# Optimization experiments

Measured on AMD Instinct MI355X. Metric: run time of the kernel, lower is better.

Reference implementation:

```python
import jax, jax.numpy as jnp
import numpy as np

B, N, E = 4, 10000, 160000
F_EXOG = 8
IN_DIM = 9          # 1 (pm25) + F_EXOG
HIST, PRED = 8, 12
HID = 64
GNN_OUT = 13
E_HID, E_OUT = 32, 30
GRU_IN = IN_DIM + GNN_OUT  # 22


def setup_inputs() -> dict:
    key = jax.random.key(0)
    ks = jax.random.split(key, 16)
    s = 0.1
    return {
        "pm25_hist": jax.random.normal(ks[0], (B, HIST, N, 1), jnp.float32),
        "feature": jax.random.normal(ks[1], (B, HIST + PRED, N, F_EXOG), jnp.float32),
        "edge_attr": jax.random.uniform(ks[2], (E, 2), jnp.float32),
        "wind_mean": jnp.array([2.0, 180.0], jnp.float32),
        "wind_std": jnp.array([1.5, 90.0], jnp.float32),
        # edge MLP: Linear(21->32), Sigmoid, Linear(32->30), Sigmoid
        "e_w1": jax.random.normal(ks[3], (2 * IN_DIM + 3, E_HID), jnp.float32) * s,
        "e_b1": jnp.zeros((E_HID,), jnp.float32),
        "e_w2": jax.random.normal(ks[4], (E_HID, E_OUT), jnp.float32) * s,
        "e_b2": jnp.zeros((E_OUT,), jnp.float32),
        # node MLP: Linear(30->13), Sigmoid
        "n_w": jax.random.normal(ks[5], (E_OUT, GNN_OUT), jnp.float32) * s,
        "n_b": jnp.zeros((GNN_OUT,), jnp.float32),
        # GRUCell(22 -> 64), torch layout: weight_ih (3H, in), weight_hh (3H, H)
        "gru_wi": jax.random.normal(ks[6], (3 * HID, GRU_IN), jnp.float32) * s,
        "gru_wh": jax.random.normal(ks[7], (3 * HID, HID), jnp.float32) * s,
        "gru_bi": jnp.zeros((3 * HID,), jnp.float32),
        "gru_bh": jnp.zeros((3 * HID,), jnp.float32),
        # fc_out: Linear(64 -> 1)
        "fc_w": jax.random.normal(ks[8], (HID, 1), jnp.float32) * s,
        "fc_b": jnp.zeros((1,), jnp.float32),
        "edge_index": jax.random.randint(ks[9], (2, E), 0, N, jnp.int64),
    }


def _forward(pm25_hist, feature, edge_attr, wind_mean, wind_std,
             e_w1, e_b1, e_w2, e_b2, n_w, n_b,
             gru_wi, gru_wh, gru_bi, gru_bh, fc_w, fc_b, edge_index):
    batch, _, n_nodes, _ = pm25_hist.shape
    src, tgt = edge_index[0], edge_index[1]

    # buffers precomputed in __init__ (torch.std uses ddof=1)
    edge_mean = edge_attr.mean(axis=0, keepdims=True)
    edge_std = jnp.maximum(jnp.std(edge_attr, axis=0, ddof=1, keepdims=True), 1e-6)
    edge_attr_norm = (edge_attr - edge_mean) / edge_std          # (E, 2)
    city_dist = jnp.maximum(edge_attr[:, 0], 1e-3)               # (E,)
    city_direc = edge_attr[:, 1]                                 # (E,)
    w_std = jnp.maximum(wind_std, 1e-6)

    def graph_gnn(x):                                            # x: (B, N, IN_DIM)
        node_src = x[:, src]                                     # (B, E, IN_DIM)
        node_tgt = x[:, tgt]
        wind = node_src[..., -2:] * w_std + wind_mean            # de-normalize
        speed = jnp.maximum(wind[..., 0], 0.0)                   # (B, E)
        wdir = jnp.deg2rad(wind[..., 1])
        theta = jnp.abs(city_direc - wdir)
        edge_w = jax.nn.relu(3.0 * speed * jnp.cos(theta) / city_dist)  # (B, E)
        ean = jnp.broadcast_to(edge_attr_norm, (x.shape[0], E, 2))
        h = jnp.concatenate([node_src, node_tgt, ean, edge_w[..., None]], axis=-1)
        h = jax.nn.sigmoid(h @ e_w1 + e_b1)
        h = jax.nn.sigmoid(h @ e_w2 + e_b2)                      # (B, E, E_OUT)
        agg = jnp.zeros((x.shape[0], n_nodes, E_OUT), x.dtype)
        agg = agg.at[:, tgt].add(h).at[:, src].add(-h)           # scatter add / sub
        return jax.nn.sigmoid(agg @ n_w + n_b)                   # (B, N, GNN_OUT)

    def gru_step(h, x):                                          # h,x: (B*N, .)
        gi = x @ gru_wi.T + gru_bi
        gh = h @ gru_wh.T + gru_bh
        i_r, i_z, i_n = jnp.split(gi, 3, axis=-1)
        h_r, h_z, h_n = jnp.split(gh, 3, axis=-1)
        r = jax.nn.sigmoid(i_r + h_r)
        z = jax.nn.sigmoid(i_z + h_z)
        n = jnp.tanh(i_n + r * h_n)
        return (1.0 - z) * n + z * h

    def step(carry, feat_t):
        hn, xn = carry                                           # (B*N,HID), (B,N,1)
        x = jnp.concatenate([xn, feat_t], axis=-1)               # (B, N, IN_DIM)
        x_gnn = graph_gnn(x)
        xc = jnp.concatenate([x_gnn, x], axis=-1).reshape(batch * n_nodes, -1)
        hn = gru_step(hn, xc)
        xn = hn.reshape(batch, n_nodes, HID) @ fc_w + fc_b       # (B, N, 1)
        return (hn, xn), xn[..., 0]

    hn0 = jnp.zeros((batch * n_nodes, HID), pm25_hist.dtype)
    xn0 = pm25_hist[:, -1]                                       # (B, N, 1)
    feats = jnp.swapaxes(feature[:, HIST:HIST + PRED], 0, 1)     # (PRED, B, N, F)
    _, preds = jax.lax.scan(step, (hn0, xn0), feats)             # (PRED, B, N)
    return jnp.transpose(preds, (1, 2, 0))                       # (B, N, PRED)


def reference(pm25_hist, feature, edge_attr, wind_mean, wind_std,
              e_w1, e_b1, e_w2, e_b2, n_w, n_b,
              gru_wi, gru_wh, gru_bi, gru_bh, fc_w, fc_b, edge_index):
    return _forward(pm25_hist, feature, edge_attr, wind_mean, wind_std,
                    e_w1, e_b1, e_w2, e_b2, n_w, n_b,
                    gru_wi, gru_wh, gru_bi, gru_bh, fc_w, fc_b, edge_index)
```

## Files before the change

### kernel.cpp

```cpp
#include <hip/hip_runtime.h>
#include <hip/hip_fp16.h>
#include <cstddef>

#define BB    4
#define NN    10000
#define EE    160000
#define BN    40000
#define HISTC 8
#define PREDC 12
#define TSTEP 20
#define FEX   8
#define HIDC  64
#define EHID  32
#define EOUTC 30
#define GOUTC 13
#define GINC  22

typedef float v2f __attribute__((ext_vector_type(2)));
typedef _Float16 v2h __attribute__((ext_vector_type(2)));

struct alignas(16) WPack {
    __half2 w[16];
    float   nw[14];
    float   b2;
    float   pad;
};

__device__ __forceinline__ float fast_rcp(float x) { return __builtin_amdgcn_rcpf(x); }
__device__ __forceinline__ float sigm(float x) {
    return fast_rcp(1.0f + __expf(-x));
}
__device__ __forceinline__ v2f sigm2(v2f x) {
    v2f r; r.x = sigm(x.x); r.y = sigm(x.y); return r;
}
__device__ __forceinline__ float tanh_fast(float x) {
    x = fminf(fmaxf(x, -15.0f), 15.0f);
    float e = __expf(2.0f * x);
    return (e - 1.0f) * fast_rcp(e + 1.0f);
}

__device__ __forceinline__ float dot2(__half2 a, __half2 b, float c) {
#if __has_builtin(__builtin_amdgcn_fdot2)
    union { __half2 h; v2h v; } ua, ub;
    ua.h = a; ub.h = b;
    return __builtin_amdgcn_fdot2(ua.v, ub.v, c, false);
#else
    float2 fa = __half22float2(a), fb = __half22float2(b);
    return c + fa.x * fb.x + fa.y * fb.y;
#endif
}

__global__ __launch_bounds__(256) void stats1_kernel(const float* __restrict__ ea,
                                                     double* __restrict__ part) {
    __shared__ double sm[256][4];
    int tid = threadIdx.x;
    double s0 = 0, s1 = 0, q0 = 0, q1 = 0;
    for (int e = blockIdx.x * 256 + tid; e < EE; e += 256 * 256) {
        float2 v = reinterpret_cast<const float2*>(ea)[e];
        double v0 = (double)v.x, v1 = (double)v.y;
        s0 += v0; q0 += v0 * v0;
        s1 += v1; q1 += v1 * v1;
    }
    sm[tid][0] = s0; sm[tid][1] = s1; sm[tid][2] = q0; sm[tid][3] = q1;
    __syncthreads();
    for (int off = 128; off > 0; off >>= 1) {
        if (tid < off)
            for (int k = 0; k < 4; k++) sm[tid][k] += sm[tid + off][k];
        __syncthreads();
    }
    if (tid == 0) {
        part[blockIdx.x * 4 + 0] = sm[0][0];
        part[blockIdx.x * 4 + 1] = sm[0][1];
        part[blockIdx.x * 4 + 2] = sm[0][2];
        part[blockIdx.x * 4 + 3] = sm[0][3];
    }
}

__global__ __launch_bounds__(256) void stats2_kernel(const double* __restrict__ part,
                                                     float* __restrict__ stats) {
    __shared__ double sm[256][4];
    int tid = threadIdx.x;
    sm[tid][0] = part[tid * 4 + 0];
    sm[tid][1] = part[tid * 4 + 1];
    sm[tid][2] = part[tid * 4 + 2];
    sm[tid][3] = part[tid * 4 + 3];
    __syncthreads();
    for (int off = 128; off > 0; off >>= 1) {
        if (tid < off)
            for (int k = 0; k < 4; k++) sm[tid][k] += sm[tid + off][k];
        __syncthreads();
    }
    if (tid == 0) {
        double m0 = sm[0][0] / EE, m1 = sm[0][1] / EE;
        double v0 = (sm[0][2] - sm[0][0] * sm[0][0] / EE) / (double)(EE - 1);
        double v1 = (sm[0][3] - sm[0][1] * sm[0][1] / EE) / (double)(EE - 1);
        float sd0 = fmaxf((float)sqrt(v0 > 0 ? v0 : 0.0), 1e-6f);
        float sd1 = fmaxf((float)sqrt(v1 > 0 ? v1 : 0.0), 1e-6f);
        stats[0] = (float)m0; stats[1] = (float)m1;
        stats[2] = 1.0f / sd0; stats[3] = 1.0f / sd1;
    }
}

__global__ __launch_bounds__(256) void edgepre_kernel(
    const float* __restrict__ ea, const float* __restrict__ stats,
    const int* __restrict__ eidx,
    int* __restrict__ deg_t, int* __restrict__ deg_s,
    float4* __restrict__ epre4)
{
    int e = blockIdx.x * 256 + threadIdx.x;
    if (e >= EE) return;
    float2 v = reinterpret_cast<const float2*>(ea)[e];
    float4 r;
    r.x = (v.x - stats[0]) * stats[2];
    r.y = (v.y - stats[1]) * stats[3];
    r.z = 1.0f / fmaxf(v.x, 1e-3f);
    r.w = v.y;
    epre4[e] = r;
    atomicAdd(&deg_s[eidx[e]], 1);
    atomicAdd(&deg_t[eidx[EE + e]], 1);
}

__global__ __launch_bounds__(256) void cvtw_kernel(
    const float* __restrict__ wi, const float* __restrict__ wh,
    const float* __restrict__ ew2, const float* __restrict__ eb2,
    const float* __restrict__ nw,
    __half* __restrict__ wi_h, __half* __restrict__ wh_h,
    WPack* __restrict__ wpack)
{
    int i = blockIdx.x * 256 + threadIdx.x;
    if (i < 192 * GINC) wi_h[i] = __float2half(wi[i]);
    if (i < 192 * HIDC) wh_h[i] = __float2half(wh[i]);
    if (i < EOUTC) {
        WPack wp;
        #pragma unroll
        for (int q = 0; q < 16; q++)
            wp.w[q] = __floats2half2_rn(ew2[(2 * q) * EOUTC + i],
                                        ew2[(2 * q + 1) * EOUTC + i]);
        #pragma unroll
        for (int j = 0; j < GOUTC; j++) wp.nw[j] = nw[i * GOUTC + j];
        wp.nw[13] = 0.f;
        wp.b2 = eb2[i];
        wp.pad = 0.f;
        wpack[i] = wp;
    }
}

__global__ void initxn_kernel(const float* __restrict__ pm, float* __restrict__ xn) {
    int i = blockIdx.x * 256 + threadIdx.x;
    if (i >= BN) return;
    int b = i / NN, n = i - b * NN;
    xn[i] = pm[(b * HISTC + (HISTC - 1)) * NN + n];
}

__global__ __launch_bounds__(1024) void scan_kernel(
    const int* __restrict__ deg_t, const int* __restrict__ deg_s,
    int* __restrict__ off_t, int* __restrict__ off_s,
    int* __restrict__ cnt_t, int* __restrict__ cnt_s)
{
    __shared__ int pt[1024], ps[1024];
    int tid = threadIdx.x;
    int base = tid * 10;
    int st = 0, ss = 0;
    for (int k = 0; k < 10; k++) {
        int i = base + k;
        if (i < NN) { st += deg_t[i]; ss += deg_s[i]; }
    }
    pt[tid] = st; ps[tid] = ss;
    __syncthreads();
    for (int off = 1; off < 1024; off <<= 1) {
        int vt = (tid >= off) ? pt[tid - off] : 0;
        int vs = (tid >= off) ? ps[tid - off] : 0;
        __syncthreads();
        pt[tid] += vt; ps[tid] += vs;
        __syncthreads();
    }
    int ext = (tid == 0) ? 0 : pt[tid - 1];
    int exs = (tid == 0) ? 0 : ps[tid - 1];
    for (int k = 0; k < 10; k++) {
        int i = base + k;
        if (i < NN) {
            off_t[i] = ext; cnt_t[i] = ext;
            off_s[i] = exs; cnt_s[i] = exs;
            ext += deg_t[i]; exs += deg_s[i];
        }
    }
    if (tid == 0) { off_t[NN] = EE; off_s[NN] = EE; }
}

__global__ void fillperm_kernel(const int* __restrict__ eidx,
                                const float4* __restrict__ epre4,
                                int* __restrict__ cnt_t, int* __restrict__ cnt_s,
                                int4* __restrict__ eT, float4* __restrict__ epreT)
{
    int e = blockIdx.x * 256 + threadIdx.x;
    if (e >= EE) return;
    int s = eidx[e];
    int g = eidx[EE + e];
    int pt = atomicAdd(&cnt_t[g], 1);
    int ps = atomicAdd(&cnt_s[s], 1);
    int4 r; r.x = s; r.y = g; r.z = ps; r.w = 0;
    eT[pt] = r;
    epreT[pt] = epre4[e];
}

__global__ __launch_bounds__(256) void pre_kernel(
    float* __restrict__ xncur, const float* __restrict__ feature, int t,
    const float* __restrict__ xp,
    const float* __restrict__ fb,
    const float* __restrict__ ew1,
    const float* __restrict__ wmean, const float* __restrict__ wstd,
    __half* __restrict__ preS, __half* __restrict__ preT,
    float2* __restrict__ wind2, float* __restrict__ out)
{
    __shared__ alignas(16) float w1s[18 * EHID];
    for (int i = threadIdx.x; i < 18 * EHID; i += 256) w1s[i] = ew1[i];
    __syncthreads();
    int idx = blockIdx.x * 256 + threadIdx.x;
    if (idx >= BN * 8) return;
    int i = idx >> 3;
    int c = idx & 7;
    int b = i / NN, n = i - b * NN;
    float x0;
    if (t == 0) {
        x0 = xncur[i];
    } else {
        x0 = (xp[i] + xp[BN + i]) + (xp[2 * BN + i] + xp[3 * BN + i]) + fb[0];
        if (c == 0) {
            xncur[i] = x0;
            out[(size_t)i * PREDC + (t - 1)] = x0;
        }
    }
    float x[9];
    x[0] = x0;
    {
        const float4* fp = reinterpret_cast<const float4*>(
            feature + (((size_t)b * TSTEP + HISTC + t) * NN + n) * FEX);
        float4 u = fp[0], v = fp[1];
        x[1] = u.x; x[2] = u.y; x[3] = u.z; x[4] = u.w;
        x[5] = v.x; x[6] = v.y; x[7] = v.z; x[8] = v.w;
    }
    float4 aS = {0.f, 0.f, 0.f, 0.f}, aT = {0.f, 0.f, 0.f, 0.f};
    #pragma unroll
    for (int k = 0; k < 9; k++) {
        float4 wS = reinterpret_cast<const float4*>(&w1s[k * EHID])[c];
        float4 wT = reinterpret_cast<const float4*>(&w1s[(9 + k) * EHID])[c];
        aS.x += x[k] * wS.x; aS.y += x[k] * wS.y; aS.z += x[k] * wS.z; aS.w += x[k] * wS.w;
        aT.x += x[k] * wT.x; aT.y += x[k] * wT.y; aT.z += x[k] * wT.z; aT.w += x[k] * wT.w;
    }
    union { uint2 u; __half h[4]; } sv, tv;
    sv.h[0] = __float2half(aS.x); sv.h[1] = __float2half(aS.y);
    sv.h[2] = __float2half(aS.z); sv.h[3] = __float2half(aS.w);
    tv.h[0] = __float2half(aT.x); tv.h[1] = __float2half(aT.y);
    tv.h[2] = __float2half(aT.z); tv.h[3] = __float2half(aT.w);
    reinterpret_cast<uint2*>(preS + (size_t)i * EHID)[c] = sv.u;
    reinterpret_cast<uint2*>(preT + (size_t)i * EHID)[c] = tv.u;
    if (c == 1) {
        float sd0 = fmaxf(wstd[0], 1e-6f), sd1 = fmaxf(wstd[1], 1e-6f);
        float speed = fmaxf(x[7] * sd0 + wmean[0], 0.f);
        float wdir  = (x[8] * sd1 + wmean[1]) * 0.017453292519943295f;
        float2 wv; wv.x = 3.0f * speed; wv.y = wdir;
        wind2[i] = wv;
    }
}

__global__ __launch_bounds__(256) void finalout_kernel(
    const float* __restrict__ xp, const float* __restrict__ fb,
    float* __restrict__ out)
{
    int i = blockIdx.x * 256 + threadIdx.x;
    if (i >= BN) return;
    out[(size_t)i * PREDC + (PREDC - 1)] =
        (xp[i] + xp[BN + i]) + (xp[2 * BN + i] + xp[3 * BN + i]) + fb[0];
}

__global__ __launch_bounds__(256) void edge_kernel(
    const int4* __restrict__ eT, const float4* __restrict__ epreT,
    const __half* __restrict__ preS, const __half* __restrict__ preT,
    const float2* __restrict__ wind2,
    const float* __restrict__ ew1, const float* __restrict__ eb1,
    const WPack* __restrict__ wpack,
    __half* __restrict__ h3t, __half* __restrict__ h3s)
{
    int i = blockIdx.x * 256 + threadIdx.x;
    int b = blockIdx.y;
    int4 et = eT[i];
    int s = et.x, g = et.y, ps = et.z;
    float4 ep = epreT[i];

    size_t iS = (size_t)b * NN + s, iT = (size_t)b * NN + g;
    float2 wv2 = wind2[iS];
    float ew = fmaxf(wv2.x * __cosf(fabsf(ep.w - wv2.y)) * ep.z, 0.f);

    union alignas(16) { uint4 u[4]; __half2 h2[16]; } RS, RT;
    {
        const uint4* p;
        p = reinterpret_cast<const uint4*>(preS + iS * EHID);
        RS.u[0] = p[0]; RS.u[1] = p[1]; RS.u[2] = p[2]; RS.u[3] = p[3];
        p = reinterpret_cast<const uint4*>(preT + iT * EHID);
        RT.u[0] = p[0]; RT.u[1] = p[1]; RT.u[2] = p[2]; RT.u[3] = p[3];
    }

    const v2f* W18 = reinterpret_cast<const v2f*>(ew1 + 18 * EHID);
    const v2f* W19 = reinterpret_cast<const v2f*>(ew1 + 19 * EHID);
    const v2f* W20 = reinterpret_cast<const v2f*>(ew1 + 20 * EHID);
    const v2f* B1  = reinterpret_cast<const v2f*>(eb1);
    float ean0 = ep.x, ean1 = ep.y;
    __half2 h1h[16];
    #pragma unroll
    for (int q = 0; q < 16; q++) {
        v2f u = W18[q] * ean0 + W19[q] * ean1 + B1[q] + W20[q] * ew;
        float2 rs = __half22float2(RS.h2[q]);
        float2 rt = __half22float2(RT.h2[q]);
        u.x += rs.x + rt.x;
        u.y += rs.y + rt.y;
        v2f sg = sigm2(u);
        h1h[q] = __floats2half2_rn(sg.x, sg.y);
    }

    v2f h3p[7];
    #pragma unroll
    for (int j = 0; j < 7; j++) { h3p[j].x = 0.f; h3p[j].y = 0.f; }
    for (int o = 0; o < EOUTC; o++) {
        const WPack* W = wpack + o;
        float acc0 = W->b2, acc1 = 0.f;
        #pragma unroll
        for (int q = 0; q < 16; q += 2) {
            acc0 = dot2(h1h[q],     W->w[q],     acc0);
            acc1 = dot2(h1h[q + 1], W->w[q + 1], acc1);
        }
        float h2v = sigm(acc0 + acc1);
        const v2f* nr = reinterpret_cast<const v2f*>(W->nw);
        #pragma unroll
        for (int j = 0; j < 7; j++) h3p[j] += nr[j] * h2v;
    }

    union alignas(16) { uint4 u[2]; __half2 h2[8]; } r;
    #pragma unroll
    for (int j = 0; j < 7; j++) r.h2[j] = __floats2half2_rn(h3p[j].x, h3p[j].y);
    r.h2[7] = __floats2half2_rn(0.f, 0.f);
    {
        __half* oT = h3t + ((size_t)b * EE + i) * 16;
        reinterpret_cast<uint4*>(oT)[0] = r.u[0];
        reinterpret_cast<uint4*>(oT)[1] = r.u[1];
        __half* oS = h3s + ((size_t)b * EE + ps) * 16;
        reinterpret_cast<uint4*>(oS)[0] = r.u[0];
        reinterpret_cast<uint4*>(oS)[1] = r.u[1];
    }
}

__global__ __launch_bounds__(256) void gather_kernel(
    const __half* __restrict__ h3t, const __half* __restrict__ h3s,
    const int* __restrict__ off_t, const int* __restrict__ off_s,
    const float* __restrict__ nb, const float* __restrict__ xncur,
    __half* __restrict__ xcagg)
{
    int n = (blockIdx.x * 256 + threadIdx.x) >> 6;
    if (n >= NN) return;
    n = __builtin_amdgcn_readfirstlane(n);
    int lane = threadIdx.x & 63;
    int b = lane >> 4, ch = lane & 15;
    const __half* ht = h3t + (size_t)b * EE * 16 + ch;
    const __half* hs = h3s + (size_t)b * EE * 16 + ch;
    float a0 = 0.f, a1 = 0.f, a2 = 0.f, a3 = 0.f;
    {
        int i0 = off_t[n], i1 = off_t[n + 1];
        int i = i0;
        for (; i + 4 <= i1; i += 4) {
            a0 += __half2float(ht[(size_t)(i + 0) * 16]);
            a1 += __half2float(ht[(size_t)(i + 1) * 16]);
            a2 += __half2float(ht[(size_t)(i + 2) * 16]);
            a3 += __half2float(ht[(size_t)(i + 3) * 16]);
        }
        for (; i < i1; i++) a0 += __half2float(ht[(size_t)i * 16]);
    }
    {
        int i0 = off_s[n], i1 = off_s[n + 1];
        int i = i0;
        for (; i + 4 <= i1; i += 4) {
            a0 -= __half2float(hs[(size_t)(i + 0) * 16]);
            a1 -= __half2float(hs[(size_t)(i + 1) * 16]);
            a2 -= __half2float(hs[(size_t)(i + 2) * 16]);
            a3 -= __half2float(hs[(size_t)(i + 3) * 16]);
        }
        for (; i < i1; i++) a0 -= __half2float(hs[(size_t)i * 16]);
    }
    float acc = (a0 + a1) + (a2 + a3);
    float val;
    if (ch < GOUTC) {
        val = sigm(acc + nb[ch]);
    } else if (ch == GOUTC) {
        val = xncur[(size_t)b * NN + n];
    } else {
        val = 0.f;
    }
    xcagg[((size_t)b * NN + n) * 16 + ch] = __float2half(val);
}

__global__ __launch_bounds__(256) void node_kernel(
    const __half* __restrict__ xcagg, const float* __restrict__ feature, int t,
    const __half* __restrict__ wi_h, const __half* __restrict__ wh_h,
    const float* __restrict__ bi, const float* __restrict__ bh,
    const float* __restrict__ fw,
    const __half2* __restrict__ hnold, __half2* __restrict__ hnnew,
    float* __restrict__ xp)
{
    __shared__ float xpart[4][64];
    int lane = threadIdx.x & 63;
    int wav  = threadIdx.x >> 6;
    int jb   = blockIdx.y;
    int node = blockIdx.x * 64 + lane;
    int b = node / NN;
    int n = node - b * NN;

    __half2 xch[11];
    {
        union alignas(16) { uint4 u[2]; __half2 h2[8]; } X;
        const uint4* xp16 = reinterpret_cast<const uint4*>(xcagg + (size_t)node * 16);
        X.u[0] = xp16[0]; X.u[1] = xp16[1];
        #pragma unroll
        for (int p = 0; p < 7; p++) xch[p] = X.h2[p];
    }
    {
        const float4* fp = reinterpret_cast<const float4*>(
            feature + (((size_t)b * TSTEP + HISTC + t) * NN + n) * FEX);
        float4 u = fp[0], v = fp[1];
        xch[7]  = __floats2half2_rn(u.x, u.y);
        xch[8]  = __floats2half2_rn(u.z, u.w);
        xch[9]  = __floats2half2_rn(v.x, v.y);
        xch[10] = __floats2half2_rn(v.z, v.w);
    }

    __half2 hh[32];
    #pragma unroll
    for (int p = 0; p < 32; p++) hh[p] = hnold[(size_t)p * BN + node];

    float xsum = 0.f;
    #pragma unroll
    for (int jj2 = 0; jj2 < 2; jj2++) {
        int j0 = __builtin_amdgcn_readfirstlane(jb * 16 + wav * 4 + jj2 * 2);
        union { __half2 h; __half v[2]; } holdw;
        holdw.h = hnold[(size_t)(j0 >> 1) * BN + node];
        float hnew2[2];
        #pragma unroll
        for (int d = 0; d < 2; d++) {
            int j = j0 + d;
            float ir = bi[j], iz = bi[64 + j], in_ = bi[128 + j];
            const __half2* wr0 = reinterpret_cast<const __half2*>(wi_h + (size_t)j * GINC);
            const __half2* wr1 = reinterpret_cast<const __half2*>(wi_h + (size_t)(64 + j) * GINC);
            const __half2* wr2 = reinterpret_cast<const __half2*>(wi_h + (size_t)(128 + j) * GINC);
            #pragma unroll
            for (int p = 0; p < 11; p++) {
                ir  = dot2(xch[p], wr0[p], ir);
                iz  = dot2(xch[p], wr1[p], iz);
                in_ = dot2(xch[p], wr2[p], in_);
            }
            float hr0 = bh[j], hz0 = bh[64 + j], hn0 = bh[128 + j];
            float hr1 = 0.f, hz1 = 0.f, hn1 = 0.f;
            const __half2* vr0 = reinterpret_cast<const __half2*>(wh_h + (size_t)j * HIDC);
            const __half2* vr1 = reinterpret_cast<const __half2*>(wh_h + (size_t)(64 + j) * HIDC);
            const __half2* vr2 = reinterpret_cast<const __half2*>(wh_h + (size_t)(128 + j) * HIDC);
            #pragma unroll
            for (int p = 0; p < 32; p += 2) {
                hr0 = dot2(hh[p],     vr0[p],     hr0);
                hz0 = dot2(hh[p],     vr1[p],     hz0);
                hn0 = dot2(hh[p],     vr2[p],     hn0);
                hr1 = dot2(hh[p + 1], vr0[p + 1], hr1);
                hz1 = dot2(hh[p + 1], vr1[p + 1], hz1);
                hn1 = dot2(hh[p + 1], vr2[p + 1], hn1);
            }
            float r  = sigm(ir + hr0 + hr1);
            float z  = sigm(iz + hz0 + hz1);
            float nn = tanh_fast(in_ + r * (hn0 + hn1));
            float hold = __half2float(holdw.v[d]);
            float hnew = (1.f - z) * nn + z * hold;
            hnew2[d] = hnew;
            xsum += hnew * fw[j];
        }
        hnnew[(size_t)(j0 >> 1) * BN + node] = __floats2half2_rn(hnew2[0], hnew2[1]);
    }
    xpart[wav][lane] = xsum;
    __syncthreads();
    if (wav == 0) {
        float tot = xpart[0][lane] + xpart[1][lane] + xpart[2][lane] + xpart[3][lane];
        xp[(size_t)jb * BN + node] = tot;
    }
}

extern "C" void kernel_launch(void* const* d_in, const int* in_sizes, int n_in,
                              void* d_out, int out_size, void* d_ws, size_t ws_size,
                              hipStream_t stream)
{
    const float* pm    = (const float*)d_in[0];
    const float* feat  = (const float*)d_in[1];
    const float* ea    = (const float*)d_in[2];
    const float* wmean = (const float*)d_in[3];
    const float* wstd  = (const float*)d_in[4];
    const float* ew1   = (const float*)d_in[5];
    const float* eb1   = (const float*)d_in[6];
    const float* ew2   = (const float*)d_in[7];
    const float* eb2   = (const float*)d_in[8];
    const float* nw    = (const float*)d_in[9];
    const float* nb    = (const float*)d_in[10];
    const float* wi    = (const float*)d_in[11];
    const float* wh    = (const float*)d_in[12];
    const float* bi    = (const float*)d_in[13];
    const float* bh    = (const float*)d_in[14];
    const float* fw    = (const float*)d_in[15];
    const float* fb    = (const float*)d_in[16];
    const int*   eidx  = (const int*)d_in[17];
    float* out = (float*)d_out;

    char* w = (char*)d_ws;
    double* partd = (double*)w;                    w += 256 * 4 * sizeof(double);
    float*  stats = (float*)w;                     w += 16 * sizeof(float);
    WPack*  wpack = (WPack*)w;                     w += EOUTC * sizeof(WPack);
    float4* epre4 = (float4*)w;                    w += (size_t)EE * sizeof(float4);
    float4* epreT = (float4*)w;                    w += (size_t)EE * sizeof(float4);
    float*  xncur = (float*)w;                     w += (size_t)BN * sizeof(float);
    float*  xp    = (float*)w;                     w += (size_t)4 * BN * sizeof(float);
    __half2* hnA  = (__half2*)w;                   w += (size_t)32 * BN * sizeof(__half2);
    __half2* hnB  = (__half2*)w;                   w += (size_t)32 * BN * sizeof(__half2);
    __half* xcagg = (__half*)w;                    w += (size_t)BN * 16 * sizeof(__half);
    __half* preS  = (__half*)w;                    w += (size_t)BN * EHID * sizeof(__half);
    __half* preT  = (__half*)w;                    w += (size_t)BN * EHID * sizeof(__half);
    float2* wind2 = (float2*)w;                    w += (size_t)BN * sizeof(float2);
    __half* h3t   = (__half*)w;                    w += (size_t)BB * EE * 16 * sizeof(__half);
    __half* h3s   = (__half*)w;                    w += (size_t)BB * EE * 16 * sizeof(__half);
    __half* wi_h  = (__half*)w;                    w += (size_t)192 * GINC * sizeof(__half);
    __half* wh_h  = (__half*)w;                    w += (size_t)192 * HIDC * sizeof(__half);
    int*    deg_t = (int*)w;                       w += NN * sizeof(int);
    int*    deg_s = (int*)w;                       w += NN * sizeof(int);
    int*    off_t = (int*)w;                       w += (NN + 1) * sizeof(int);
    int*    off_s = (int*)w;                       w += (NN + 1) * sizeof(int);
    int*    cnt_t = (int*)w;                       w += NN * sizeof(int);
    int*    cnt_s = (int*)w;                       w += NN * sizeof(int);
    int4*   eT    = (int4*)w;                      w += (size_t)EE * sizeof(int4);

    stats1_kernel<<<256, 256, 0, stream>>>(ea, partd);
    stats2_kernel<<<1, 256, 0, stream>>>(partd, stats);
    hipMemsetAsync(deg_t, 0, 2 * NN * sizeof(int), stream);
    edgepre_kernel<<<(EE + 255) / 256, 256, 0, stream>>>(
        ea, stats, eidx, deg_t, deg_s, epre4);
    cvtw_kernel<<<(192 * HIDC + 255) / 256, 256, 0, stream>>>(
        wi, wh, ew2, eb2, nw, wi_h, wh_h, wpack);
    initxn_kernel<<<(BN + 255) / 256, 256, 0, stream>>>(pm, xncur);
    hipMemsetAsync(hnA, 0, (size_t)32 * BN * sizeof(__half2), stream);
    scan_kernel<<<1, 1024, 0, stream>>>(deg_t, deg_s, off_t, off_s, cnt_t, cnt_s);
    fillperm_kernel<<<(EE + 255) / 256, 256, 0, stream>>>(
        eidx, epre4, cnt_t, cnt_s, eT, epreT);

    for (int t = 0; t < PREDC; t++) {
        const __half2* hnold = (t & 1) ? hnB : hnA;
        __half2*       hnnew = (t & 1) ? hnA : hnB;
        pre_kernel<<<(BN * 8 + 255) / 256, 256, 0, stream>>>(
            xncur, feat, t, xp, fb, ew1, wmean, wstd, preS, preT, wind2, out);
        edge_kernel<<<dim3(EE / 256, BB), 256, 0, stream>>>(
            eT, epreT, preS, preT, wind2, ew1, eb1, wpack, h3t, h3s);
        gather_kernel<<<(NN * 64 + 255) / 256, 256, 0, stream>>>(
            h3t, h3s, off_t, off_s, nb, xncur, xcagg);
        node_kernel<<<dim3(BN / 64, 4), 256, 0, stream>>>(
            xcagg, feat, t, wi_h, wh_h, bi, bh, fw, hnold, hnnew, xp);
    }
    finalout_kernel<<<(BN + 255) / 256, 256, 0, stream>>>(xp, fb, out);
}
```

Baseline: 1.046 ms.

## Precompute feature edge-MLP terms for all steps and fuse gather with GRU node step

```diff
diff --git a/kernel.cpp b/kernel.cpp
--- a/kernel.cpp
+++ b/kernel.cpp
@@ -203,80 +203,61 @@
     epreT[pt] = epre4[e];
 }
 
-__global__ __launch_bounds__(256) void pre_kernel(
-    float* __restrict__ xncur, const float* __restrict__ feature, int t,
-    const float* __restrict__ xp,
-    const float* __restrict__ fb,
+__global__ __launch_bounds__(256) void featpre_kernel(
+    const float* __restrict__ feature,
     const float* __restrict__ ew1,
     const float* __restrict__ wmean, const float* __restrict__ wstd,
-    __half* __restrict__ preS, __half* __restrict__ preT,
-    float2* __restrict__ wind2, float* __restrict__ out)
+    __half* __restrict__ preSfeat, __half* __restrict__ preTfeat,
+    float2* __restrict__ wind2all)
 {
     __shared__ alignas(16) float w1s[18 * EHID];
     for (int i = threadIdx.x; i < 18 * EHID; i += 256) w1s[i] = ew1[i];
     __syncthreads();
     int idx = blockIdx.x * 256 + threadIdx.x;
-    if (idx >= BN * 8) return;
-    int i = idx >> 3;
-    int c = idx & 7;
+    if (idx >= BN * 8 * PREDC) return;
+    int c  = idx & 7;
+    int r2 = idx >> 3;
+    int t  = r2 / BN;
+    int i  = r2 - t * BN;
     int b = i / NN, n = i - b * NN;
-    float x0;
-    if (t == 0) {
-        x0 = xncur[i];
-    } else {
-        x0 = (xp[i] + xp[BN + i]) + (xp[2 * BN + i] + xp[3 * BN + i]) + fb[0];
-        if (c == 0) {
-            xncur[i] = x0;
-            out[(size_t)i * PREDC + (t - 1)] = x0;
-        }
-    }
-    float x[9];
-    x[0] = x0;
+    float xf[8];
     {
         const float4* fp = reinterpret_cast<const float4*>(
             feature + (((size_t)b * TSTEP + HISTC + t) * NN + n) * FEX);
         float4 u = fp[0], v = fp[1];
-        x[1] = u.x; x[2] = u.y; x[3] = u.z; x[4] = u.w;
-        x[5] = v.x; x[6] = v.y; x[7] = v.z; x[8] = v.w;
+        xf[0] = u.x; xf[1] = u.y; xf[2] = u.z; xf[3] = u.w;
+        xf[4] = v.x; xf[5] = v.y; xf[6] = v.z; xf[7] = v.w;
     }
     float4 aS = {0.f, 0.f, 0.f, 0.f}, aT = {0.f, 0.f, 0.f, 0.f};
     #pragma unroll
-    for (int k = 0; k < 9; k++) {
-        float4 wS = reinterpret_cast<const float4*>(&w1s[k * EHID])[c];
-        float4 wT = reinterpret_cast<const float4*>(&w1s[(9 + k) * EHID])[c];
-        aS.x += x[k] * wS.x; aS.y += x[k] * wS.y; aS.z += x[k] * wS.z; aS.w += x[k] * wS.w;
-        aT.x += x[k] * wT.x; aT.y += x[k] * wT.y; aT.z += x[k] * wT.z; aT.w += x[k] * wT.w;
+    for (int k = 0; k < 8; k++) {
+        float4 wS = reinterpret_cast<const float4*>(&w1s[(k + 1) * EHID])[c];
+        float4 wT = reinterpret_cast<const float4*>(&w1s[(10 + k) * EHID])[c];
+        aS.x += xf[k] * wS.x; aS.y += xf[k] * wS.y; aS.z += xf[k] * wS.z; aS.w += xf[k] * wS.w;
+        aT.x += xf[k] * wT.x; aT.y += xf[k] * wT.y; aT.z += xf[k] * wT.z; aT.w += xf[k] * wT.w;
     }
     union { uint2 u; __half h[4]; } sv, tv;
     sv.h[0] = __float2half(aS.x); sv.h[1] = __float2half(aS.y);
     sv.h[2] = __float2half(aS.z); sv.h[3] = __float2half(aS.w);
     tv.h[0] = __float2half(aT.x); tv.h[1] = __float2half(aT.y);
     tv.h[2] = __float2half(aT.z); tv.h[3] = __float2half(aT.w);
-    reinterpret_cast<uint2*>(preS + (size_t)i * EHID)[c] = sv.u;
-    reinterpret_cast<uint2*>(preT + (size_t)i * EHID)[c] = tv.u;
+    size_t base = ((size_t)t * BN + i) * EHID;
+    reinterpret_cast<uint2*>(preSfeat + base)[c] = sv.u;
+    reinterpret_cast<uint2*>(preTfeat + base)[c] = tv.u;
     if (c == 1) {
         float sd0 = fmaxf(wstd[0], 1e-6f), sd1 = fmaxf(wstd[1], 1e-6f);
-        float speed = fmaxf(x[7] * sd0 + wmean[0], 0.f);
-        float wdir  = (x[8] * sd1 + wmean[1]) * 0.017453292519943295f;
+        float speed = fmaxf(xf[6] * sd0 + wmean[0], 0.f);
+        float wdir  = (xf[7] * sd1 + wmean[1]) * 0.017453292519943295f;
         float2 wv; wv.x = 3.0f * speed; wv.y = wdir;
-        wind2[i] = wv;
-    }
-}
-
-__global__ __launch_bounds__(256) void finalout_kernel(
-    const float* __restrict__ xp, const float* __restrict__ fb,
-    float* __restrict__ out)
-{
-    int i = blockIdx.x * 256 + threadIdx.x;
-    if (i >= BN) return;
-    out[(size_t)i * PREDC + (PREDC - 1)] =
-        (xp[i] + xp[BN + i]) + (xp[2 * BN + i] + xp[3 * BN + i]) + fb[0];
+        wind2all[(size_t)t * BN + i] = wv;
+    }
 }
 
 __global__ __launch_bounds__(256) void edge_kernel(
     const int4* __restrict__ eT, const float4* __restrict__ epreT,
-    const __half* __restrict__ preS, const __half* __restrict__ preT,
-    const float2* __restrict__ wind2,
+    const __half* __restrict__ preSfeat, const __half* __restrict__ preTfeat,
+    const float2* __restrict__ wind2all, int t,
+    const float* __restrict__ xncur,
     const float* __restrict__ ew1, const float* __restrict__ eb1,
     const WPack* __restrict__ wpack,
     __half* __restrict__ h3t, __half* __restrict__ h3s)
@@ -288,18 +269,22 @@
     float4 ep = epreT[i];
 
     size_t iS = (size_t)b * NN + s, iT = (size_t)b * NN + g;
-    float2 wv2 = wind2[iS];
+    size_t tb = (size_t)t * BN;
+    float2 wv2 = wind2all[tb + iS];
     float ew = fmaxf(wv2.x * __cosf(fabsf(ep.w - wv2.y)) * ep.z, 0.f);
+    float xnS = xncur[iS], xnT = xncur[iT];
 
     union alignas(16) { uint4 u[4]; __half2 h2[16]; } RS, RT;
     {
         const uint4* p;
-        p = reinterpret_cast<const uint4*>(preS + iS * EHID);
+        p = reinterpret_cast<const uint4*>(preSfeat + (tb + iS) * EHID);
         RS.u[0] = p[0]; RS.u[1] = p[1]; RS.u[2] = p[2]; RS.u[3] = p[3];
-        p = reinterpret_cast<const uint4*>(preT + iT * EHID);
+        p = reinterpret_cast<const uint4*>(preTfeat + (tb + iT) * EHID);
         RT.u[0] = p[0]; RT.u[1] = p[1]; RT.u[2] = p[2]; RT.u[3] = p[3];
     }
 
+    const v2f* W00 = reinterpret_cast<const v2f*>(ew1);
+    const v2f* W09 = reinterpret_cast<const v2f*>(ew1 + 9 * EHID);
     const v2f* W18 = reinterpret_cast<const v2f*>(ew1 + 18 * EHID);
     const v2f* W19 = reinterpret_cast<const v2f*>(ew1 + 19 * EHID);
     const v2f* W20 = reinterpret_cast<const v2f*>(ew1 + 20 * EHID);
@@ -308,7 +293,8 @@
     __half2 h1h[16];
     #pragma unroll
     for (int q = 0; q < 16; q++) {
-        v2f u = W18[q] * ean0 + W19[q] * ean1 + B1[q] + W20[q] * ew;
+        v2f u = W18[q] * ean0 + W19[q] * ean1 + B1[q] + W20[q] * ew
+              + W00[q] * xnS + W09[q] * xnT;
         float2 rs = __half22float2(RS.h2[q]);
         float2 rt = __half22float2(RT.h2[q]);
         u.x += rs.x + rt.x;
@@ -348,81 +334,77 @@
     }
 }
 
-__global__ __launch_bounds__(256) void gather_kernel(
+__global__ __launch_bounds__(256) void gathernode_kernel(
     const __half* __restrict__ h3t, const __half* __restrict__ h3s,
     const int* __restrict__ off_t, const int* __restrict__ off_s,
-    const float* __restrict__ nb, const float* __restrict__ xncur,
-    __half* __restrict__ xcagg)
-{
-    int n = (blockIdx.x * 256 + threadIdx.x) >> 6;
-    if (n >= NN) return;
-    n = __builtin_amdgcn_readfirstlane(n);
-    int lane = threadIdx.x & 63;
-    int b = lane >> 4, ch = lane & 15;
-    const __half* ht = h3t + (size_t)b * EE * 16 + ch;
-    const __half* hs = h3s + (size_t)b * EE * 16 + ch;
-    float a0 = 0.f, a1 = 0.f, a2 = 0.f, a3 = 0.f;
-    {
-        int i0 = off_t[n], i1 = off_t[n + 1];
-        int i = i0;
-        for (; i + 4 <= i1; i += 4) {
-            a0 += __half2float(ht[(size_t)(i + 0) * 16]);
-            a1 += __half2float(ht[(size_t)(i + 1) * 16]);
-            a2 += __half2float(ht[(size_t)(i + 2) * 16]);
-            a3 += __half2float(ht[(size_t)(i + 3) * 16]);
-        }
-        for (; i < i1; i++) a0 += __half2float(ht[(size_t)i * 16]);
-    }
-    {
-        int i0 = off_s[n], i1 = off_s[n + 1];
-        int i = i0;
-        for (; i + 4 <= i1; i += 4) {
-            a0 -= __half2float(hs[(size_t)(i + 0) * 16]);
-            a1 -= __half2float(hs[(size_t)(i + 1) * 16]);
-            a2 -= __half2float(hs[(size_t)(i + 2) * 16]);
-            a3 -= __half2float(hs[(size_t)(i + 3) * 16]);
-        }
-        for (; i < i1; i++) a0 -= __half2float(hs[(size_t)i * 16]);
-    }
-    float acc = (a0 + a1) + (a2 + a3);
-    float val;
-    if (ch < GOUTC) {
-        val = sigm(acc + nb[ch]);
-    } else if (ch == GOUTC) {
-        val = xncur[(size_t)b * NN + n];
-    } else {
-        val = 0.f;
-    }
-    xcagg[((size_t)b * NN + n) * 16 + ch] = __float2half(val);
-}
-
-__global__ __launch_bounds__(256) void node_kernel(
-    const __half* __restrict__ xcagg, const float* __restrict__ feature, int t,
+    const float* __restrict__ nb,
+    const float* __restrict__ feature, int t,
     const __half* __restrict__ wi_h, const __half* __restrict__ wh_h,
     const float* __restrict__ bi, const float* __restrict__ bh,
-    const float* __restrict__ fw,
+    const float* __restrict__ fw, const float* __restrict__ fb,
     const __half2* __restrict__ hnold, __half2* __restrict__ hnnew,
-    float* __restrict__ xp)
-{
+    float* __restrict__ xncur, float* __restrict__ out)
+{
+    __shared__ alignas(16) __half xcs[16][4][16];
     __shared__ float xpart[4][64];
-    int lane = threadIdx.x & 63;
-    int wav  = threadIdx.x >> 6;
-    int jb   = blockIdx.y;
-    int node = blockIdx.x * 64 + lane;
-    int b = node / NN;
-    int n = node - b * NN;
+    int tid = threadIdx.x;
+    int n0 = blockIdx.x * 16;
+
+    {
+        int l = tid & 63;
+        int gb = l >> 4, ch = l & 15;
+        int wv = tid >> 6;
+        const __half* ht = h3t + (size_t)gb * ((size_t)EE * 16) + ch;
+        const __half* hs = h3s + (size_t)gb * ((size_t)EE * 16) + ch;
+        for (int rr = 0; rr < 4; rr++) {
+            int ln = rr * 4 + wv;
+            int n = __builtin_amdgcn_readfirstlane(n0 + ln);
+            float a0 = 0.f, a1 = 0.f, a2 = 0.f, a3 = 0.f;
+            {
+                int i0 = off_t[n], i1 = off_t[n + 1];
+                int i = i0;
+                for (; i + 4 <= i1; i += 4) {
+                    a0 += __half2float(ht[(size_t)(i + 0) * 16]);
+                    a1 += __half2float(ht[(size_t)(i + 1) * 16]);
+                    a2 += __half2float(ht[(size_t)(i + 2) * 16]);
+                    a3 += __half2float(ht[(size_t)(i + 3) * 16]);
+                }
+                for (; i < i1; i++) a0 += __half2float(ht[(size_t)i * 16]);
+            }
+            {
+                int i0 = off_s[n], i1 = off_s[n + 1];
+                int i = i0;
+                for (; i + 4 <= i1; i += 4) {
+                    a0 -= __half2float(hs[(size_t)(i + 0) * 16]);
+                    a1 -= __half2float(hs[(size_t)(i + 1) * 16]);
+                    a2 -= __half2float(hs[(size_t)(i + 2) * 16]);
+                    a3 -= __half2float(hs[(size_t)(i + 3) * 16]);
+                }
+                for (; i < i1; i++) a0 -= __half2float(hs[(size_t)i * 16]);
+            }
+            float acc = (a0 + a1) + (a2 + a3);
+            __half v = (ch < GOUTC) ? __float2half(sigm(acc + nb[ch]))
+                                    : __float2half(0.f);
+            xcs[ln][gb][ch] = v;
+        }
+    }
+    __syncthreads();
+
+    int lane = tid & 63, wav = tid >> 6;
+    int nn = lane & 15, b = lane >> 4;
+    int node = b * NN + n0 + nn;
+    float xn_old = xncur[node];
 
     __half2 xch[11];
     {
-        union alignas(16) { uint4 u[2]; __half2 h2[8]; } X;
-        const uint4* xp16 = reinterpret_cast<const uint4*>(xcagg + (size_t)node * 16);
-        X.u[0] = xp16[0]; X.u[1] = xp16[1];
+        const __half2* xp2 = reinterpret_cast<const __half2*>(&xcs[nn][b][0]);
         #pragma unroll
-        for (int p = 0; p < 7; p++) xch[p] = X.h2[p];
+        for (int p = 0; p < 6; p++) xch[p] = xp2[p];
+        xch[6] = __halves2half2(xcs[nn][b][12], __float2half(xn_old));
     }
     {
         const float4* fp = reinterpret_cast<const float4*>(
-            feature + (((size_t)b * TSTEP + HISTC + t) * NN + n) * FEX);
+            feature + (((size_t)b * TSTEP + HISTC + t) * NN + (n0 + nn)) * FEX);
         float4 u = fp[0], v = fp[1];
         xch[7]  = __floats2half2_rn(u.x, u.y);
         xch[8]  = __floats2half2_rn(u.z, u.w);
@@ -435,54 +417,58 @@
     for (int p = 0; p < 32; p++) hh[p] = hnold[(size_t)p * BN + node];
 
     float xsum = 0.f;
-    #pragma unroll
-    for (int jj2 = 0; jj2 < 2; jj2++) {
-        int j0 = __builtin_amdgcn_readfirstlane(jb * 16 + wav * 4 + jj2 * 2);
-        union { __half2 h; __half v[2]; } holdw;
-        holdw.h = hnold[(size_t)(j0 >> 1) * BN + node];
-        float hnew2[2];
+    for (int jb = 0; jb < 4; jb++) {
         #pragma unroll
-        for (int d = 0; d < 2; d++) {
-            int j = j0 + d;
-            float ir = bi[j], iz = bi[64 + j], in_ = bi[128 + j];
-            const __half2* wr0 = reinterpret_cast<const __half2*>(wi_h + (size_t)j * GINC);
-            const __half2* wr1 = reinterpret_cast<const __half2*>(wi_h + (size_t)(64 + j) * GINC);
-            const __half2* wr2 = reinterpret_cast<const __half2*>(wi_h + (size_t)(128 + j) * GINC);
+        for (int jj2 = 0; jj2 < 2; jj2++) {
+            int j0 = __builtin_amdgcn_readfirstlane(jb * 16 + wav * 4 + jj2 * 2);
+            union { __half2 h; __half v[2]; } holdw;
+            holdw.h = hnold[(size_t)(j0 >> 1) * BN + node];
+            float hnew2[2];
             #pragma unroll
-            for (int p = 0; p < 11; p++) {
-                ir  = dot2(xch[p], wr0[p], ir);
-                iz  = dot2(xch[p], wr1[p], iz);
-                in_ = dot2(xch[p], wr2[p], in_);
+            for (int d = 0; d < 2; d++) {
+                int j = j0 + d;
+                float ir = bi[j], iz = bi[64 + j], in_ = bi[128 + j];
+                const __half2* wr0 = reinterpret_cast<const __half2*>(wi_h + (size_t)j * GINC);
+                const __half2* wr1 = reinterpret_cast<const __half2*>(wi_h + (size_t)(64 + j) * GINC);
+                const __half2* wr2 = reinterpret_cast<const __half2*>(wi_h + (size_t)(128 + j) * GINC);
+                #pragma unroll
+                for (int p = 0; p < 11; p++) {
+                    ir  = dot2(xch[p], wr0[p], ir);
+                    iz  = dot2(xch[p], wr1[p], iz);
+                    in_ = dot2(xch[p], wr2[p], in_);
+                }
+                float hr0 = bh[j], hz0 = bh[64 + j], hn0 = bh[128 + j];
+                float hr1 = 0.f, hz1 = 0.f, hn1 = 0.f;
+                const __half2* vr0 = reinterpret_cast<const __half2*>(wh_h + (size_t)j * HIDC);
+                const __half2* vr1 = reinterpret_cast<const __half2*>(wh_h + (size_t)(64 + j) * HIDC);
+                const __half2* vr2 = reinterpret_cast<const __half2*>(wh_h + (size_t)(128 + j) * HIDC);
+                #pragma unroll
+                for (int p = 0; p < 32; p += 2) {
+                    hr0 = dot2(hh[p],     vr0[p],     hr0);
+                    hz0 = dot2(hh[p],     vr1[p],     hz0);
+                    hn0 = dot2(hh[p],     vr2[p],     hn0);
+                    hr1 = dot2(hh[p + 1], vr0[p + 1], hr1);
+                    hz1 = dot2(hh[p + 1], vr1[p + 1], hz1);
+                    hn1 = dot2(hh[p + 1], vr2[p + 1], hn1);
+                }
+                float r  = sigm(ir + hr0 + hr1);
+                float z  = sigm(iz + hz0 + hz1);
+                float nl = tanh_fast(in_ + r * (hn0 + hn1));
+                float hold = __half2float(holdw.v[d]);
+                float hnew = (1.f - z) * nl + z * hold;
+                hnew2[d] = hnew;
+                xsum += hnew * fw[j];
             }
-            float hr0 = bh[j], hz0 = bh[64 + j], hn0 = bh[128 + j];
-            float hr1 = 0.f, hz1 = 0.f, hn1 = 0.f;
-            const __half2* vr0 = reinterpret_cast<const __half2*>(wh_h + (size_t)j * HIDC);
-            const __half2* vr1 = reinterpret_cast<const __half2*>(wh_h + (size_t)(64 + j) * HIDC);
-            const __half2* vr2 = reinterpret_cast<const __half2*>(wh_h + (size_t)(128 + j) * HIDC);
-            #pragma unroll
-            for (int p = 0; p < 32; p += 2) {
-                hr0 = dot2(hh[p],     vr0[p],     hr0);
-                hz0 = dot2(hh[p],     vr1[p],     hz0);
-                hn0 = dot2(hh[p],     vr2[p],     hn0);
-                hr1 = dot2(hh[p + 1], vr0[p + 1], hr1);
-                hz1 = dot2(hh[p + 1], vr1[p + 1], hz1);
-                hn1 = dot2(hh[p + 1], vr2[p + 1], hn1);
-            }
-            float r  = sigm(ir + hr0 + hr1);
-            float z  = sigm(iz + hz0 + hz1);
-            float nn = tanh_fast(in_ + r * (hn0 + hn1));
-            float hold = __half2float(holdw.v[d]);
-            float hnew = (1.f - z) * nn + z * hold;
-            hnew2[d] = hnew;
-            xsum += hnew * fw[j];
+            hnnew[(size_t)(j0 >> 1) * BN + node] = __floats2half2_rn(hnew2[0], hnew2[1]);
         }
-        hnnew[(size_t)(j0 >> 1) * BN + node] = __floats2half2_rn(hnew2[0], hnew2[1]);
     }
     xpart[wav][lane] = xsum;
     __syncthreads();
     if (wav == 0) {
         float tot = xpart[0][lane] + xpart[1][lane] + xpart[2][lane] + xpart[3][lane];
-        xp[(size_t)jb * BN + node] = tot;
+        float xnew = tot + fb[0];
+        xncur[node] = xnew;
+        out[(size_t)node * PREDC + t] = xnew;
     }
 }
 
@@ -517,24 +503,22 @@
     float4* epre4 = (float4*)w;                    w += (size_t)EE * sizeof(float4);
     float4* epreT = (float4*)w;                    w += (size_t)EE * sizeof(float4);
     float*  xncur = (float*)w;                     w += (size_t)BN * sizeof(float);
-    float*  xp    = (float*)w;                     w += (size_t)4 * BN * sizeof(float);
     __half2* hnA  = (__half2*)w;                   w += (size_t)32 * BN * sizeof(__half2);
     __half2* hnB  = (__half2*)w;                   w += (size_t)32 * BN * sizeof(__half2);
-    __half* xcagg = (__half*)w;                    w += (size_t)BN * 16 * sizeof(__half);
-    __half* preS  = (__half*)w;                    w += (size_t)BN * EHID * sizeof(__half);
-    __half* preT  = (__half*)w;                    w += (size_t)BN * EHID * sizeof(__half);
-    float2* wind2 = (float2*)w;                    w += (size_t)BN * sizeof(float2);
+    __half* preSfeat = (__half*)w;                 w += (size_t)PREDC * BN * EHID * sizeof(__half);
+    __half* preTfeat = (__half*)w;                 w += (size_t)PREDC * BN * EHID * sizeof(__half);
+    float2* wind2all = (float2*)w;                 w += (size_t)PREDC * BN * sizeof(float2);
     __half* h3t   = (__half*)w;                    w += (size_t)BB * EE * 16 * sizeof(__half);
     __half* h3s   = (__half*)w;                    w += (size_t)BB * EE * 16 * sizeof(__half);
     __half* wi_h  = (__half*)w;                    w += (size_t)192 * GINC * sizeof(__half);
     __half* wh_h  = (__half*)w;                    w += (size_t)192 * HIDC * sizeof(__half);
+    int4*   eT    = (int4*)w;                      w += (size_t)EE * sizeof(int4);
     int*    deg_t = (int*)w;                       w += NN * sizeof(int);
     int*    deg_s = (int*)w;                       w += NN * sizeof(int);
     int*    off_t = (int*)w;                       w += (NN + 1) * sizeof(int);
     int*    off_s = (int*)w;                       w += (NN + 1) * sizeof(int);
     int*    cnt_t = (int*)w;                       w += NN * sizeof(int);
     int*    cnt_s = (int*)w;                       w += NN * sizeof(int);
-    int4*   eT    = (int4*)w;                      w += (size_t)EE * sizeof(int4);
 
     stats1_kernel<<<256, 256, 0, stream>>>(ea, partd);
     stats2_kernel<<<1, 256, 0, stream>>>(partd, stats);
@@ -548,18 +532,17 @@
     scan_kernel<<<1, 1024, 0, stream>>>(deg_t, deg_s, off_t, off_s, cnt_t, cnt_s);
     fillperm_kernel<<<(EE + 255) / 256, 256, 0, stream>>>(
         eidx, epre4, cnt_t, cnt_s, eT, epreT);
+    featpre_kernel<<<(BN * 8 * PREDC + 255) / 256, 256, 0, stream>>>(
+        feat, ew1, wmean, wstd, preSfeat, preTfeat, wind2all);
 
     for (int t = 0; t < PREDC; t++) {
         const __half2* hnold = (t & 1) ? hnB : hnA;
         __half2*       hnnew = (t & 1) ? hnA : hnB;
-        pre_kernel<<<(BN * 8 + 255) / 256, 256, 0, stream>>>(
-            xncur, feat, t, xp, fb, ew1, wmean, wstd, preS, preT, wind2, out);
         edge_kernel<<<dim3(EE / 256, BB), 256, 0, stream>>>(
-            eT, epreT, preS, preT, wind2, ew1, eb1, wpack, h3t, h3s);
-        gather_kernel<<<(NN * 64 + 255) / 256, 256, 0, stream>>>(
-            h3t, h3s, off_t, off_s, nb, xncur, xcagg);
-        node_kernel<<<dim3(BN / 64, 4), 256, 0, stream>>>(
-            xcagg, feat, t, wi_h, wh_h, bi, bh, fw, hnold, hnnew, xp);
-    }
-    finalout_kernel<<<(BN + 255) / 256, 256, 0, stream>>>(xp, fb, out);
-}
+            eT, epreT, preSfeat, preTfeat, wind2all, t, xncur,
+            ew1, eb1, wpack, h3t, h3s);
+        gathernode_kernel<<<NN / 16, 256, 0, stream>>>(
+            h3t, h3s, off_t, off_s, nb, feat, t, wi_h, wh_h, bi, bh,
+            fw, fb, hnold, hnnew, xncur, out);
+    }
+}
```

Measured after the change: 1.145 ms. 1.09x slower.

## Fuse GRU hidden-unit split into one 1024-thread block with fc_out reduction

Applied to the files above, without the earlier changes.

```diff
diff --git a/kernel.cpp b/kernel.cpp
--- a/kernel.cpp
+++ b/kernel.cpp
@@ -204,13 +204,11 @@
 }
 
 __global__ __launch_bounds__(256) void pre_kernel(
-    float* __restrict__ xncur, const float* __restrict__ feature, int t,
-    const float* __restrict__ xp,
-    const float* __restrict__ fb,
+    const float* __restrict__ xncur, const float* __restrict__ feature, int t,
     const float* __restrict__ ew1,
     const float* __restrict__ wmean, const float* __restrict__ wstd,
     __half* __restrict__ preS, __half* __restrict__ preT,
-    float2* __restrict__ wind2, float* __restrict__ out)
+    float2* __restrict__ wind2)
 {
     __shared__ alignas(16) float w1s[18 * EHID];
     for (int i = threadIdx.x; i < 18 * EHID; i += 256) w1s[i] = ew1[i];
@@ -220,18 +218,8 @@
     int i = idx >> 3;
     int c = idx & 7;
     int b = i / NN, n = i - b * NN;
-    float x0;
-    if (t == 0) {
-        x0 = xncur[i];
-    } else {
-        x0 = (xp[i] + xp[BN + i]) + (xp[2 * BN + i] + xp[3 * BN + i]) + fb[0];
-        if (c == 0) {
-            xncur[i] = x0;
-            out[(size_t)i * PREDC + (t - 1)] = x0;
-        }
-    }
     float x[9];
-    x[0] = x0;
+    x[0] = xncur[i];
     {
         const float4* fp = reinterpret_cast<const float4*>(
             feature + (((size_t)b * TSTEP + HISTC + t) * NN + n) * FEX);
@@ -261,16 +249,6 @@
         float2 wv; wv.x = 3.0f * speed; wv.y = wdir;
         wind2[i] = wv;
     }
-}
-
-__global__ __launch_bounds__(256) void finalout_kernel(
-    const float* __restrict__ xp, const float* __restrict__ fb,
-    float* __restrict__ out)
-{
-    int i = blockIdx.x * 256 + threadIdx.x;
-    if (i >= BN) return;
-    out[(size_t)i * PREDC + (PREDC - 1)] =
-        (xp[i] + xp[BN + i]) + (xp[2 * BN + i] + xp[3 * BN + i]) + fb[0];
 }
 
 __global__ __launch_bounds__(256) void edge_kernel(
@@ -396,19 +374,28 @@
     xcagg[((size_t)b * NN + n) * 16 + ch] = __float2half(val);
 }
 
-__global__ __launch_bounds__(256) void node_kernel(
+__global__ __launch_bounds__(1024, 8) void node_kernel(
     const __half* __restrict__ xcagg, const float* __restrict__ feature, int t,
     const __half* __restrict__ wi_h, const __half* __restrict__ wh_h,
     const float* __restrict__ bi, const float* __restrict__ bh,
-    const float* __restrict__ fw,
+    const float* __restrict__ fw, const float* __restrict__ fb,
     const __half2* __restrict__ hnold, __half2* __restrict__ hnnew,
-    float* __restrict__ xp)
-{
-    __shared__ float xpart[4][64];
-    int lane = threadIdx.x & 63;
-    int wav  = threadIdx.x >> 6;
-    int jb   = blockIdx.y;
-    int node = blockIdx.x * 64 + lane;
+    float* __restrict__ xncur, float* __restrict__ out)
+{
+    __shared__ __half2 shh[32][65];
+    __shared__ float xpart[16][64];
+    int tid  = threadIdx.x;
+    int lane = tid & 63;
+    int wav  = tid >> 6;
+    int g0   = blockIdx.x * 64;
+
+    for (int k = tid; k < 32 * 64; k += 1024) {
+        int p = k >> 6, l = k & 63;
+        shh[p][l] = hnold[(size_t)p * BN + g0 + l];
+    }
+    __syncthreads();
+
+    int node = g0 + lane;
     int b = node / NN;
     int n = node - b * NN;
 
@@ -432,57 +419,59 @@
 
     __half2 hh[32];
     #pragma unroll
-    for (int p = 0; p < 32; p++) hh[p] = hnold[(size_t)p * BN + node];
-
+    for (int p = 0; p < 32; p++) hh[p] = shh[p][lane];
+
+    float hnew4[4];
     float xsum = 0.f;
     #pragma unroll
-    for (int jj2 = 0; jj2 < 2; jj2++) {
-        int j0 = __builtin_amdgcn_readfirstlane(jb * 16 + wav * 4 + jj2 * 2);
-        union { __half2 h; __half v[2]; } holdw;
-        holdw.h = hnold[(size_t)(j0 >> 1) * BN + node];
-        float hnew2[2];
-        #pragma unroll
-        for (int d = 0; d < 2; d++) {
-            int j = j0 + d;
-            float ir = bi[j], iz = bi[64 + j], in_ = bi[128 + j];
-            const __half2* wr0 = reinterpret_cast<const __half2*>(wi_h + (size_t)j * GINC);
-            const __half2* wr1 = reinterpret_cast<const __half2*>(wi_h + (size_t)(64 + j) * GINC);
-            const __half2* wr2 = reinterpret_cast<const __half2*>(wi_h + (size_t)(128 + j) * GINC);
-            #pragma unroll
-            for (int p = 0; p < 11; p++) {
-                ir  = dot2(xch[p], wr0[p], ir);
-                iz  = dot2(xch[p], wr1[p], iz);
-                in_ = dot2(xch[p], wr2[p], in_);
-            }
-            float hr0 = bh[j], hz0 = bh[64 + j], hn0 = bh[128 + j];
-            float hr1 = 0.f, hz1 = 0.f, hn1 = 0.f;
-            const __half2* vr0 = reinterpret_cast<const __half2*>(wh_h + (size_t)j * HIDC);
-            const __half2* vr1 = reinterpret_cast<const __half2*>(wh_h + (size_t)(64 + j) * HIDC);
-            const __half2* vr2 = reinterpret_cast<const __half2*>(wh_h + (size_t)(128 + j) * HIDC);
-            #pragma unroll
-            for (int p = 0; p < 32; p += 2) {
-                hr0 = dot2(hh[p],     vr0[p],     hr0);
-                hz0 = dot2(hh[p],     vr1[p],     hz0);
-                hn0 = dot2(hh[p],     vr2[p],     hn0);
-                hr1 = dot2(hh[p + 1], vr0[p + 1], hr1);
-                hz1 = dot2(hh[p + 1], vr1[p + 1], hz1);
-                hn1 = dot2(hh[p + 1], vr2[p + 1], hn1);
-            }
-            float r  = sigm(ir + hr0 + hr1);
-            float z  = sigm(iz + hz0 + hz1);
-            float nn = tanh_fast(in_ + r * (hn0 + hn1));
-            float hold = __half2float(holdw.v[d]);
-            float hnew = (1.f - z) * nn + z * hold;
-            hnew2[d] = hnew;
-            xsum += hnew * fw[j];
+    for (int d = 0; d < 4; d++) {
+        int j = __builtin_amdgcn_readfirstlane(wav * 4 + d);
+        float ir = bi[j], iz = bi[64 + j], in_ = bi[128 + j];
+        const __half2* wr0 = reinterpret_cast<const __half2*>(wi_h + (size_t)j * GINC);
+        const __half2* wr1 = reinterpret_cast<const __half2*>(wi_h + (size_t)(64 + j) * GINC);
+        const __half2* wr2 = reinterpret_cast<const __half2*>(wi_h + (size_t)(128 + j) * GINC);
+        #pragma unroll
+        for (int p = 0; p < 11; p++) {
+            ir  = dot2(xch[p], wr0[p], ir);
+            iz  = dot2(xch[p], wr1[p], iz);
+            in_ = dot2(xch[p], wr2[p], in_);
         }
-        hnnew[(size_t)(j0 >> 1) * BN + node] = __floats2half2_rn(hnew2[0], hnew2[1]);
-    }
+        float hr0 = bh[j], hz0 = bh[64 + j], hn0 = bh[128 + j];
+        float hr1 = 0.f, hz1 = 0.f, hn1 = 0.f;
+        const __half2* vr0 = reinterpret_cast<const __half2*>(wh_h + (size_t)j * HIDC);
+        const __half2* vr1 = reinterpret_cast<const __half2*>(wh_h + (size_t)(64 + j) * HIDC);
+        const __half2* vr2 = reinterpret_cast<const __half2*>(wh_h + (size_t)(128 + j) * HIDC);
+        #pragma unroll
+        for (int p = 0; p < 32; p += 2) {
+            hr0 = dot2(hh[p],     vr0[p],     hr0);
+            hz0 = dot2(hh[p],     vr1[p],     hz0);
+            hn0 = dot2(hh[p],     vr2[p],     hn0);
+            hr1 = dot2(hh[p + 1], vr0[p + 1], hr1);
+            hz1 = dot2(hh[p + 1], vr1[p + 1], hz1);
+            hn1 = dot2(hh[p + 1], vr2[p + 1], hn1);
+        }
+        float r  = sigm(ir + hr0 + hr1);
+        float z  = sigm(iz + hz0 + hz1);
+        float nl = tanh_fast(in_ + r * (hn0 + hn1));
+        union { __half2 h; __half v[2]; } hold2;
+        hold2.h = hh[(wav * 4 + d) >> 1];
+        float hold = __half2float(hold2.v[d & 1]);
+        float hnew = (1.f - z) * nl + z * hold;
+        hnew4[d] = hnew;
+        xsum += hnew * fw[j];
+    }
+    hnnew[(size_t)(wav * 2) * BN + node]     = __floats2half2_rn(hnew4[0], hnew4[1]);
+    hnnew[(size_t)(wav * 2 + 1) * BN + node] = __floats2half2_rn(hnew4[2], hnew4[3]);
     xpart[wav][lane] = xsum;
     __syncthreads();
-    if (wav == 0) {
-        float tot = xpart[0][lane] + xpart[1][lane] + xpart[2][lane] + xpart[3][lane];
-        xp[(size_t)jb * BN + node] = tot;
+    if (tid < 64) {
+        float tot = 0.f;
+        #pragma unroll
+        for (int w2 = 0; w2 < 16; w2++) tot += xpart[w2][tid];
+        int node2 = g0 + tid;
+        float xnew = tot + fb[0];
+        xncur[node2] = xnew;
+        out[(size_t)node2 * PREDC + t] = xnew;
     }
 }
 
@@ -517,7 +506,6 @@
     float4* epre4 = (float4*)w;                    w += (size_t)EE * sizeof(float4);
     float4* epreT = (float4*)w;                    w += (size_t)EE * sizeof(float4);
     float*  xncur = (float*)w;                     w += (size_t)BN * sizeof(float);
-    float*  xp    = (float*)w;                     w += (size_t)4 * BN * sizeof(float);
     __half2* hnA  = (__half2*)w;                   w += (size_t)32 * BN * sizeof(__half2);
     __half2* hnB  = (__half2*)w;                   w += (size_t)32 * BN * sizeof(__half2);
     __half* xcagg = (__half*)w;                    w += (size_t)BN * 16 * sizeof(__half);
@@ -528,13 +516,13 @@
     __half* h3s   = (__half*)w;                    w += (size_t)BB * EE * 16 * sizeof(__half);
     __half* wi_h  = (__half*)w;                    w += (size_t)192 * GINC * sizeof(__half);
     __half* wh_h  = (__half*)w;                    w += (size_t)192 * HIDC * sizeof(__half);
+    int4*   eT    = (int4*)w;                      w += (size_t)EE * sizeof(int4);
     int*    deg_t = (int*)w;                       w += NN * sizeof(int);
     int*    deg_s = (int*)w;                       w += NN * sizeof(int);
     int*    off_t = (int*)w;                       w += (NN + 1) * sizeof(int);
     int*    off_s = (int*)w;                       w += (NN + 1) * sizeof(int);
     int*    cnt_t = (int*)w;                       w += NN * sizeof(int);
     int*    cnt_s = (int*)w;                       w += NN * sizeof(int);
-    int4*   eT    = (int4*)w;                      w += (size_t)EE * sizeof(int4);
 
     stats1_kernel<<<256, 256, 0, stream>>>(ea, partd);
     stats2_kernel<<<1, 256, 0, stream>>>(partd, stats);
@@ -553,13 +541,13 @@
         const __half2* hnold = (t & 1) ? hnB : hnA;
         __half2*       hnnew = (t & 1) ? hnA : hnB;
         pre_kernel<<<(BN * 8 + 255) / 256, 256, 0, stream>>>(
-            xncur, feat, t, xp, fb, ew1, wmean, wstd, preS, preT, wind2, out);
+            xncur, feat, t, ew1, wmean, wstd, preS, preT, wind2);
         edge_kernel<<<dim3(EE / 256, BB), 256, 0, stream>>>(
             eT, epreT, preS, preT, wind2, ew1, eb1, wpack, h3t, h3s);
         gather_kernel<<<(NN * 64 + 255) / 256, 256, 0, stream>>>(
             h3t, h3s, off_t, off_s, nb, xncur, xcagg);
-        node_kernel<<<dim3(BN / 64, 4), 256, 0, stream>>>(
-            xcagg, feat, t, wi_h, wh_h, bi, bh, fw, hnold, hnnew, xp);
-    }
-    finalout_kernel<<<(BN + 255) / 256, 256, 0, stream>>>(xp, fb, out);
-}
+        node_kernel<<<BN / 64, 1024, 0, stream>>>(
+            xcagg, feat, t, wi_h, wh_h, bi, bh, fw, fb,
+            hnold, hnnew, xncur, out);
+    }
+}
```

Measured after the change: 1.172 ms. 12.0% more time.
